# Performance work log

Hardware: AMD Instinct MI355X
Metric: run time of the kernel (lower is better)

Reference implementation:

```python
import jax, jax.numpy as jnp
import numpy as np

EPS = 1e-5


def gcn_conv(x, src, dst, W, b, n_nodes):
    # PyG GCNConv: linear first, symmetric normalization with self-loops.
    h = x @ W  # [N, out]
    deg = jnp.zeros((n_nodes,), h.dtype).at[dst].add(1.0) + 1.0  # +1 self-loop
    dinv = deg ** -0.5
    coef = dinv[src] * dinv[dst]  # [E]
    msg = h[src] * coef[:, None]  # edge gather (memory bound)
    agg = jax.ops.segment_sum(msg, dst, num_segments=n_nodes)
    agg = agg + h * (dinv * dinv)[:, None]  # self-loop term
    return agg + b


def graph_norm(x, batch, num_graphs, w, b, alpha):
    # PyG GraphNorm: per-graph mean/std with learnable mean scale alpha.
    ones = jnp.ones((x.shape[0],), x.dtype)
    cnt = jnp.maximum(jax.ops.segment_sum(ones, batch, num_segments=num_graphs), 1.0)
    mean = jax.ops.segment_sum(x, batch, num_segments=num_graphs) / cnt[:, None]
    out = x - alpha * mean[batch]
    var = jax.ops.segment_sum(out * out, batch, num_segments=num_graphs) / cnt[:, None]
    return w * out / jnp.sqrt(var + EPS)[batch] + b


def mean_pool(x, batch, num_graphs):
    ones = jnp.ones((x.shape[0],), x.dtype)
    cnt = jnp.maximum(jax.ops.segment_sum(ones, batch, num_segments=num_graphs), 1.0)
    return jax.ops.segment_sum(x, batch, num_segments=num_graphs) / cnt[:, None]


def setup_inputs() -> dict:
    key = jax.random.key(0)
    ks = jax.random.split(key, 16)
    N, E, G = 100000, 3200000, 512
    IN, H, OUT = 7, 128, 2
    x = jax.random.normal(ks[0], (N, IN), jnp.float32)
    edge_index = jax.random.randint(ks[1], (2, E), 0, N, jnp.int64)
    batch = jnp.sort(jax.random.randint(ks[2], (N,), 0, G, jnp.int64))
    s = lambda k, sh: jax.random.normal(k, sh, jnp.float32) * 0.05
    return {
        "x": x, "edge_index": edge_index, "batch": batch, "num_graphs": G,
        "W1": s(ks[3], (IN, H)), "b1": jnp.zeros((H,), jnp.float32),
        "gn1_w": jnp.ones((H,), jnp.float32), "gn1_b": jnp.zeros((H,), jnp.float32),
        "gn1_a": jnp.ones((H,), jnp.float32),
        "W2": s(ks[4], (H, H)), "b2": jnp.zeros((H,), jnp.float32),
        "gn2_w": jnp.ones((H,), jnp.float32), "gn2_b": jnp.zeros((H,), jnp.float32),
        "gn2_a": jnp.ones((H,), jnp.float32),
        "H1": s(ks[5], (H, H)), "hb1": jnp.zeros((H,), jnp.float32),
        "H2": s(ks[6], (H, OUT)), "hb2": jnp.zeros((OUT,), jnp.float32),
    }


def reference(x, edge_index, batch, num_graphs,
              W1, b1, gn1_w, gn1_b, gn1_a,
              W2, b2, gn2_w, gn2_b, gn2_a,
              H1, hb1, H2, hb2):
    n = x.shape[0]
    src, dst = edge_index[0], edge_index[1]
    # block 1
    h = gcn_conv(x, src, dst, W1, b1, n)
    h = graph_norm(h, batch, num_graphs, gn1_w, gn1_b, gn1_a)
    h = jax.nn.relu(h)
    # block 2
    h = gcn_conv(h, src, dst, W2, b2, n)
    h = graph_norm(h, batch, num_graphs, gn2_w, gn2_b, gn2_a)
    h = jax.nn.relu(h)
    # pool + MLP head (dropout inactive at eval)
    g = mean_pool(h, batch, num_graphs)  # [G, H]
    g = jax.nn.relu(g @ H1 + hb1)
    return g @ H2 + hb2  # [G, 2]
```

## Files before the change

### kernel.cpp

```cpp
#include <hip/hip_runtime.h>
#include <hip/hip_fp16.h>

#define EPSV 1e-5f
#define HDIM 128
#define BKT_SHIFT 9
#define BKT_SIZE 512
#define CHK 8192

typedef _Float16 f16x8 __attribute__((ext_vector_type(8)));
typedef float f32x4 __attribute__((ext_vector_type(4)));


__global__ __launch_bounds__(256) void hist_pass(const int* __restrict__ dst,
                                                 int* __restrict__ histG, int E, int NB) {
    __shared__ int h[BKT_SIZE];
    int t = threadIdx.x;
    for (int i = t; i < NB; i += 256) h[i] = 0;
    __syncthreads();
    int base = blockIdx.x * CHK;
    int end = min(base + CHK, E);
    for (int e = base + t; e < end; e += 256) atomicAdd(&h[dst[e] >> BKT_SHIFT], 1);
    __syncthreads();
    for (int i = t; i < NB; i += 256) histG[(size_t)blockIdx.x * NB + i] = h[i];
}

__global__ __launch_bounds__(512) void scan_chunks(int* __restrict__ histG,
                                                   int* __restrict__ tot,
                                                   int NCHUNK, int NB) {
    __shared__ int tmp[512];
    int b = blockIdx.x, t = threadIdx.x;
    int v = (t < NCHUNK) ? histG[(size_t)t * NB + b] : 0;
    tmp[t] = v;
    __syncthreads();
    for (int off = 1; off < 512; off <<= 1) {
        int x = (t >= off) ? tmp[t - off] : 0;
        __syncthreads();
        tmp[t] += x;
        __syncthreads();
    }
    if (t < NCHUNK) histG[(size_t)t * NB + b] = tmp[t] - v;
    if (t == 511) tot[b] = tmp[511];
}

__global__ __launch_bounds__(512) void scan_tot_k(const int* __restrict__ tot,
                                                  int* __restrict__ bucketBase,
                                                  int* __restrict__ rowStart,
                                                  int NB, int N, int E) {
    __shared__ int tmp[512];
    int t = threadIdx.x;
    int v = (t < NB) ? tot[t] : 0;
    tmp[t] = v;
    __syncthreads();
    for (int off = 1; off < 512; off <<= 1) {
        int x = (t >= off) ? tmp[t - off] : 0;
        __syncthreads();
        tmp[t] += x;
        __syncthreads();
    }
    if (t < NB) bucketBase[t] = tmp[t] - v;
    if (t == NB - 1) {
        bucketBase[NB] = tmp[t];
        rowStart[N] = E;
    }
}

__global__ __launch_bounds__(256) void add_base(int* __restrict__ histG,
                                                const int* __restrict__ bucketBase,
                                                int total, int NB) {
    int i = blockIdx.x * 256 + threadIdx.x;
    if (i < total) histG[i] += bucketBase[i % NB];
}

__global__ __launch_bounds__(256) void scatter_bkt(const int* __restrict__ src,
                                                   const int* __restrict__ dst,
                                                   const int* __restrict__ chunkOff,
                                                   unsigned int* __restrict__ EP,
                                                   int E, int NB) {
    __shared__ int cur[BKT_SIZE];
    int t = threadIdx.x, c = blockIdx.x;
    for (int i = t; i < NB; i += 256) cur[i] = chunkOff[(size_t)c * NB + i];
    __syncthreads();
    int base = c * CHK, end = min(base + CHK, E);
    for (int e = base + t; e < end; e += 256) {
        int d = dst[e];
        int b = d >> BKT_SHIFT;
        int pos = atomicAdd(&cur[b], 1);
        EP[pos] = (unsigned int)src[e] | ((unsigned int)(d & (BKT_SIZE - 1)) << 23);
    }
}

__global__ __launch_bounds__(512) void bucket_csr(const unsigned int* __restrict__ EP,
                                                  const int* __restrict__ bucketBase,
                                                  int* __restrict__ rowStart,
                                                  float* __restrict__ dinv,
                                                  int* __restrict__ col, int N) {
    __shared__ int cnt[BKT_SIZE];
    __shared__ int tmp[BKT_SIZE];
    int b = blockIdx.x, t = threadIdx.x;
    int ebase = bucketBase[b], eend = bucketBase[b + 1];
    cnt[t] = 0;
    __syncthreads();
    for (int e = ebase + t; e < eend; e += 512)
        atomicAdd(&cnt[(EP[e] >> 23) & 511], 1);
    __syncthreads();
    int v = cnt[t];
    tmp[t] = v;
    __syncthreads();
    for (int off = 1; off < 512; off <<= 1) {
        int x = (t >= off) ? tmp[t - off] : 0;
        __syncthreads();
        tmp[t] += x;
        __syncthreads();
    }
    int excl = tmp[t] - v;
    int n = (b << BKT_SHIFT) + t;
    if (n < N) {
        rowStart[n] = ebase + excl;
        dinv[n] = rsqrtf((float)v + 1.0f);
    }
    __syncthreads();
    cnt[t] = ebase + excl;
    __syncthreads();
    for (int e = ebase + t; e < eend; e += 512) {
        unsigned int p = EP[e];
        int ld = (p >> 23) & 511;
        int pos = atomicAdd(&cnt[ld], 1);
        col[pos] = (int)(p & 0x7FFFFFu);
    }
}

__device__ __forceinline__ int lbound(const int* __restrict__ b, int N, int key) {
    int lo = 0, hi = N;
    while (lo < hi) {
        int mid = (lo + hi) >> 1;
        if (b[mid] < key) lo = mid + 1; else hi = mid;
    }
    return lo;
}

__global__ __launch_bounds__(256) void graph_counts(const int* __restrict__ batch,
                                                    float* __restrict__ gcnt, int N, int G) {
    int g = blockIdx.x * 256 + threadIdx.x;
    if (g < G)
        gcnt[g] = (float)(lbound(batch, N, g + 1) - lbound(batch, N, g));
}

__global__ __launch_bounds__(256) void prep_w2t(const float* __restrict__ W2,
                                                __half* __restrict__ W2t) {
    int i = blockIdx.x * 256 + threadIdx.x;
    if (i < HDIM * HDIM) {
        int c = i >> 7, k = i & 127;
        W2t[c * HDIM + k] = __float2half(W2[k * HDIM + c]);
    }
}

__global__ __launch_bounds__(256) void prep_xs(const float* __restrict__ x,
                                               const float* __restrict__ dinv,
                                               float* __restrict__ xs, long long total) {
    long long idx = (long long)blockIdx.x * 256 + threadIdx.x;
    if (idx >= total) return;
    int n = (int)(idx >> 3), k = (int)(idx & 7);
    xs[idx] = (k < 7) ? x[(long long)n * 7 + k] * dinv[n] : 0.f;
}

__global__ __launch_bounds__(256) void agg7k(const int* __restrict__ col,
                                             const int* __restrict__ rowStart,
                                             const float* __restrict__ xs,
                                             float* __restrict__ agg, int N) {
    int wib = threadIdx.x >> 6, lane = threadIdx.x & 63;
    int stream = lane >> 2;
    int c2 = (lane & 3) * 2;
    int n = blockIdx.x * 4 + wib;
    if (n >= N) return;
    float2 acc = make_float2(0.f, 0.f);
    int rs = rowStart[n], re = rowStart[n + 1];
    if (stream == 0) acc = *(const float2*)(xs + (size_t)n * 8 + c2);
    int j = rs + stream;
    for (; j + 16 < re; j += 32) {
        int e0 = col[j], e1 = col[j + 16];
        float2 r0 = *(const float2*)(xs + (size_t)e0 * 8 + c2);
        float2 r1 = *(const float2*)(xs + (size_t)e1 * 8 + c2);
        acc.x += r0.x + r1.x;
        acc.y += r0.y + r1.y;
    }
    for (; j < re; j += 16) {
        float2 r = *(const float2*)(xs + (size_t)col[j] * 8 + c2);
        acc.x += r.x; acc.y += r.y;
    }
#pragma unroll
    for (int off = 4; off <= 32; off <<= 1) {
        acc.x += __shfl_xor(acc.x, off);
        acc.y += __shfl_xor(acc.y, off);
    }
    if (stream == 0) *(float2*)(agg + (size_t)n * 8 + c2) = acc;
}

__global__ __launch_bounds__(512) void l1post(const float* __restrict__ agg,
                                              const float* __restrict__ W1,
                                              const float* __restrict__ b1,
                                              const float* __restrict__ dinv,
                                              __half* __restrict__ A16, int N) {
    __shared__ float w1s[7 * HDIM];
    int t = threadIdx.x;
    for (int i = t; i < 7 * HDIM; i += 512) w1s[i] = W1[i];
    int wib = t >> 7, c = t & 127;
    int n = blockIdx.x * 4 + wib;
    __syncthreads();
    if (n < N) {
        const float* ar = agg + (size_t)n * 8;
        float s = 0.f;
#pragma unroll
        for (int k = 0; k < 7; k++) s += ar[k] * w1s[k * HDIM + c];
        A16[(size_t)n * HDIM + c] = __float2half(s * dinv[n] + b1[c]);
    }
}

__global__ __launch_bounds__(256) void stats2(const __half* __restrict__ X,
                                              const int* __restrict__ batch,
                                              float* __restrict__ gsum,
                                              float* __restrict__ gsq, int N) {
    int t = threadIdx.x;
    int c = t & 127;
    int half_ = t >> 7;
    int n0 = blockIdx.x * 32;
    float s = 0.f, q = 0.f;
    int cur = -1;
    for (int i = half_; i < 32; i += 2) {
        int n = n0 + i;
        if (n >= N) break;
        int b = batch[n];
        if (b != cur) {
            if (cur >= 0) {
                unsafeAtomicAdd(&gsum[(size_t)cur * HDIM + c], s);
                unsafeAtomicAdd(&gsq[(size_t)cur * HDIM + c], q);
            }
            cur = b; s = 0.f; q = 0.f;
        }
        float v = __half2float(X[(size_t)n * HDIM + c]);
        s += v; q += v * v;
    }
    if (cur >= 0) {
        unsafeAtomicAdd(&gsum[(size_t)cur * HDIM + c], s);
        unsafeAtomicAdd(&gsq[(size_t)cur * HDIM + c], q);
    }
}

__global__ __launch_bounds__(256) void gstat(float* __restrict__ gsum,
                                             float* __restrict__ gsq,
                                             const float* __restrict__ gcnt,
                                             const float* __restrict__ alpha, int total) {
    int i = blockIdx.x * 256 + threadIdx.x;
    if (i < total) {
        int g = i >> 7, c = i & 127;
        float cnt = fmaxf(gcnt[g], 1.f);
        float mean = gsum[i] / cnt;
        float m2 = gsq[i] / cnt;
        float a = alpha[c];
        float var = m2 + mean * mean * (a * a - 2.f * a);
        gsum[i] = mean;
        gsq[i] = rsqrtf(fmaxf(var, 0.f) + EPSV);
    }
}

__global__ __launch_bounds__(256) void mm_h_mfma(const __half* __restrict__ A16,
                                                 const float* __restrict__ gmean,
                                                 const float* __restrict__ gistd,
                                                 const float* __restrict__ alpha,
                                                 const float* __restrict__ w,
                                                 const float* __restrict__ bb,
                                                 const int* __restrict__ batch,
                                                 const __half* __restrict__ W2t,
                                                 const float* __restrict__ dinv,
                                                 __half* __restrict__ Q, int N) {
    __shared__ _Float16 XS[64][136];
    __shared__ _Float16 WT[HDIM][136];
    __shared__ float pA[HDIM], pW[HDIM], pB[HDIM];
    int t = threadIdx.x;
    for (int i = t; i < HDIM; i += 256) { pA[i] = alpha[i]; pW[i] = w[i]; pB[i] = bb[i]; }
    int n0 = blockIdx.x * 64;

    for (int i = t; i < HDIM * 16; i += 256) {
        int row = i >> 4;
        int kk = (i & 15) * 8;
        *(uint4*)&WT[row][kk] = *(const uint4*)(W2t + (size_t)row * HDIM + kk);
    }
    __syncthreads();

    for (int i = t; i < 64 * 16; i += 256) {
        int nn = i >> 4;
        int kk = (i & 15) * 8;
        int gn = n0 + nn;
        __half hv[8];
#pragma unroll
        for (int k = 0; k < 8; k++) hv[k] = __float2half(0.f);
        if (gn < N) {
            uint4 u = *(const uint4*)(A16 + (size_t)gn * HDIM + kk);
            int b = batch[gn];
            const float* mp = gmean + (size_t)b * HDIM + kk;
            const float* ip = gistd + (size_t)b * HDIM + kk;
            float2 f0 = __half22float2(*(__half2*)&u.x);
            float2 f1 = __half22float2(*(__half2*)&u.y);
            float2 f2 = __half22float2(*(__half2*)&u.z);
            float2 f3 = __half22float2(*(__half2*)&u.w);
            float f[8] = {f0.x, f0.y, f1.x, f1.y, f2.x, f2.y, f3.x, f3.y};
#pragma unroll
            for (int k = 0; k < 8; k++) {
                int c = kk + k;
                hv[k] = __float2half(fmaxf(pW[c] * (f[k] - pA[c] * mp[k]) * ip[k] + pB[c], 0.f));
            }
        }
        *(uint4*)&XS[nn][kk] = *(uint4*)hv;
    }
    __syncthreads();

    int wid = t >> 6, lane = t & 63;
    int m0 = wid * 16;
    int rlane = lane & 15;
    int kgrp = lane >> 4;
    f32x4 acc[8];
#pragma unroll
    for (int ct = 0; ct < 8; ct++) acc[ct] = (f32x4){0.f, 0.f, 0.f, 0.f};

#pragma unroll
    for (int kt = 0; kt < 4; ++kt) {
        int kbase = kt * 32 + kgrp * 8;
        f16x8 a = *(const f16x8*)&XS[m0 + rlane][kbase];
#pragma unroll
        for (int ct = 0; ct < 8; ++ct) {
            f16x8 bfr = *(const f16x8*)&WT[ct * 16 + rlane][kbase];
            acc[ct] = __builtin_amdgcn_mfma_f32_16x16x32_f16(a, bfr, acc[ct], 0, 0, 0);
        }
    }

    int rgrp = lane >> 4;
    float dv[4];
    int gnr[4];
#pragma unroll
    for (int r = 0; r < 4; r++) {
        gnr[r] = n0 + m0 + rgrp * 4 + r;
        dv[r] = (gnr[r] < N) ? dinv[gnr[r]] : 0.f;
    }
#pragma unroll
    for (int ct = 0; ct < 8; ++ct) {
#pragma unroll
        for (int r = 0; r < 4; ++r) {
            if (gnr[r] < N)
                Q[(size_t)gnr[r] * HDIM + ct * 16 + rlane] = __float2half(acc[ct][r] * dv[r]);
        }
    }
}

__device__ __forceinline__ float4 qrow4(const __half* __restrict__ Q, int e, int c4) {
    uint2 u = *(const uint2*)(Q + (size_t)e * HDIM + c4);
    float2 f0 = __half22float2(*(__half2*)&u.x);
    float2 f1 = __half22float2(*(__half2*)&u.y);
    return make_float4(f0.x, f0.y, f1.x, f1.y);
}

__global__ __launch_bounds__(256) void node_agg2(const int* __restrict__ col,
                                                 const int* __restrict__ rowStart,
                                                 const __half* __restrict__ Q,
                                                 const float* __restrict__ dinv,
                                                 const float* __restrict__ bias,
                                                 __half* __restrict__ A2, int N) {
    int wib = threadIdx.x >> 6;
    int lane = threadIdx.x & 63;
    int half = lane >> 5;
    int l = lane & 31;
    int c4 = l * 4;
    int n = blockIdx.x * 4 + wib;
    if (n >= N) return;
    float4 acc = make_float4(0.f, 0.f, 0.f, 0.f);
    int rs = rowStart[n], re = rowStart[n + 1];
    if (half == 0) acc = qrow4(Q, n, c4);
    int j = rs + half;
    for (; j + 14 < re; j += 16) {
        int e0 = col[j],      e1 = col[j + 2],  e2 = col[j + 4],  e3 = col[j + 6];
        int e4 = col[j + 8],  e5 = col[j + 10], e6 = col[j + 12], e7 = col[j + 14];
        float4 r0 = qrow4(Q, e0, c4);
        float4 r1 = qrow4(Q, e1, c4);
        float4 r2 = qrow4(Q, e2, c4);
        float4 r3 = qrow4(Q, e3, c4);
        float4 r4 = qrow4(Q, e4, c4);
        float4 r5 = qrow4(Q, e5, c4);
        float4 r6 = qrow4(Q, e6, c4);
        float4 r7 = qrow4(Q, e7, c4);
        acc.x += ((r0.x + r1.x) + (r2.x + r3.x)) + ((r4.x + r5.x) + (r6.x + r7.x));
        acc.y += ((r0.y + r1.y) + (r2.y + r3.y)) + ((r4.y + r5.y) + (r6.y + r7.y));
        acc.z += ((r0.z + r1.z) + (r2.z + r3.z)) + ((r4.z + r5.z) + (r6.z + r7.z));
        acc.w += ((r0.w + r1.w) + (r2.w + r3.w)) + ((r4.w + r5.w) + (r6.w + r7.w));
    }
    for (; j + 6 < re; j += 8) {
        int e0 = col[j], e1 = col[j + 2], e2 = col[j + 4], e3 = col[j + 6];
        float4 r0 = qrow4(Q, e0, c4);
        float4 r1 = qrow4(Q, e1, c4);
        float4 r2 = qrow4(Q, e2, c4);
        float4 r3 = qrow4(Q, e3, c4);
        acc.x += (r0.x + r1.x) + (r2.x + r3.x);
        acc.y += (r0.y + r1.y) + (r2.y + r3.y);
        acc.z += (r0.z + r1.z) + (r2.z + r3.z);
        acc.w += (r0.w + r1.w) + (r2.w + r3.w);
    }
    for (; j < re; j += 2) {
        float4 r = qrow4(Q, col[j], c4);
        acc.x += r.x; acc.y += r.y; acc.z += r.z; acc.w += r.w;
    }
    acc.x += __shfl_xor(acc.x, 32);
    acc.y += __shfl_xor(acc.y, 32);
    acc.z += __shfl_xor(acc.z, 32);
    acc.w += __shfl_xor(acc.w, 32);
    if (half == 0) {
        float dv = dinv[n];
        acc.x = acc.x * dv + bias[c4];
        acc.y = acc.y * dv + bias[c4 + 1];
        acc.z = acc.z * dv + bias[c4 + 2];
        acc.w = acc.w * dv + bias[c4 + 3];
        __half2 o0 = __floats2half2_rn(acc.x, acc.y);
        __half2 o1 = __floats2half2_rn(acc.z, acc.w);
        uint2 u;
        u.x = *(unsigned int*)&o0;
        u.y = *(unsigned int*)&o1;
        *(uint2*)(A2 + (size_t)n * HDIM + c4) = u;
    }
}

__global__ __launch_bounds__(256) void node_norm_pool(const __half* __restrict__ A2,
                                                      const float* __restrict__ gmean,
                                                      const float* __restrict__ gistd,
                                                      const float* __restrict__ alpha,
                                                      const float* __restrict__ w,
                                                      const float* __restrict__ bb,
                                                      const int* __restrict__ batch,
                                                      float* __restrict__ gpool, int N) {
    int t = threadIdx.x;
    int c = t & 127;
    int half_ = t >> 7;
    int n0 = blockIdx.x * 32;
    float ac = alpha[c], wc = w[c], bc = bb[c];
    float s = 0.f, mc = 0.f, ic = 0.f;
    int cur = -1;
    for (int i = half_; i < 32; i += 2) {
        int n = n0 + i;
        if (n >= N) break;
        int b = batch[n];
        if (b != cur) {
            if (cur >= 0) unsafeAtomicAdd(&gpool[(size_t)cur * HDIM + c], s);
            cur = b; s = 0.f;
            mc = gmean[(size_t)b * HDIM + c];
            ic = gistd[(size_t)b * HDIM + c];
        }
        float v = __half2float(A2[(size_t)n * HDIM + c]);
        s += fmaxf(wc * (v - ac * mc) * ic + bc, 0.f);
    }
    if (cur >= 0) unsafeAtomicAdd(&gpool[(size_t)cur * HDIM + c], s);
}

__global__ __launch_bounds__(128) void head(const float* __restrict__ gpool,
                                            const float* __restrict__ gcnt,
                                            const float* __restrict__ H1,
                                            const float* __restrict__ hb1,
                                            const float* __restrict__ H2,
                                            const float* __restrict__ hb2,
                                            float* __restrict__ out, int G) {
    __shared__ float gv[HDIM];
    __shared__ float tv[HDIM];
    __shared__ float r0[HDIM], r1[HDIM];
    int g = blockIdx.x;
    int c = threadIdx.x;
    float cnt = fmaxf(gcnt[g], 1.0f);
    gv[c] = gpool[(long long)g * HDIM + c] / cnt;
    __syncthreads();
    float s = hb1[c];
    for (int k = 0; k < HDIM; k++) s += gv[k] * H1[k * HDIM + c];
    tv[c] = fmaxf(s, 0.f);
    __syncthreads();
    r0[c] = tv[c] * H2[c * 2 + 0];
    r1[c] = tv[c] * H2[c * 2 + 1];
    __syncthreads();
    for (int off = 64; off > 0; off >>= 1) {
        if (c < off) { r0[c] += r0[c + off]; r1[c] += r1[c + off]; }
        __syncthreads();
    }
    if (c == 0) {
        out[(long long)g * 2 + 0] = r0[0] + hb2[0];
        out[(long long)g * 2 + 1] = r1[0] + hb2[1];
    }
}

extern "C" void kernel_launch(void* const* d_in, const int* in_sizes, int n_in,
                              void* d_out, int out_size, void* d_ws, size_t ws_size,
                              hipStream_t stream) {
    const float* x    = (const float*)d_in[0];
    const int*   ei   = (const int*)d_in[1];
    const int*   batch= (const int*)d_in[2];
    const float* W1   = (const float*)d_in[4];
    const float* b1   = (const float*)d_in[5];
    const float* gn1w = (const float*)d_in[6];
    const float* gn1b = (const float*)d_in[7];
    const float* gn1a = (const float*)d_in[8];
    const float* W2   = (const float*)d_in[9];
    const float* b2   = (const float*)d_in[10];
    const float* gn2w = (const float*)d_in[11];
    const float* gn2b = (const float*)d_in[12];
    const float* gn2a = (const float*)d_in[13];
    const float* H1   = (const float*)d_in[14];
    const float* hb1  = (const float*)d_in[15];
    const float* H2   = (const float*)d_in[16];
    const float* hb2  = (const float*)d_in[17];

    int N = in_sizes[0] / 7;
    int E = in_sizes[1] / 2;
    int G = out_size / 2;
    const int* srcI = ei;
    const int* dstI = ei + E;

    int NB = (N + BKT_SIZE - 1) >> BKT_SHIFT;
    int NCHUNK = (E + CHK - 1) / CHK;

    __half* A16   = (__half*)d_ws;
    __half* A2    = A16;
    __half* Q16   = A16 + (size_t)N * HDIM;
    float*  xs    = (float*)(Q16 + (size_t)N * HDIM);
    float*  agg   = xs + (size_t)N * 8;
    float*  gsum1 = agg + (size_t)N * 8;
    float*  gsq1  = gsum1 + (size_t)G * HDIM;
    float*  gsum2 = gsq1 + (size_t)G * HDIM;
    float*  gsq2  = gsum2 + (size_t)G * HDIM;
    float*  gpool = gsq2 + (size_t)G * HDIM;
    float*  gcnt  = gpool + (size_t)G * HDIM;
    float*  dinv  = gcnt + G;
    int* rowStart = (int*)(dinv + N);
    unsigned int* EP = (unsigned int*)(rowStart + N + 2);
    int* col      = (int*)(EP + E);
    int* histG    = col + E;
    int* tot      = histG + (size_t)NCHUNK * NB;
    int* bucketBase = tot + NB + 2;
    __half* W2t   = (__half*)(bucketBase + NB + 2);

    int gridNW = (N + 3) / 4;
    int gridGH = (G * HDIM + 255) / 256;
    int gridMM = (N + 63) / 64;
    int gridNS = (N + 31) / 32;

    hipMemsetAsync(gsum1, 0, (size_t)G * HDIM * 5 * 4, stream);

    hist_pass<<<NCHUNK, 256, 0, stream>>>(dstI, histG, E, NB);
    scan_chunks<<<NB, 512, 0, stream>>>(histG, tot, NCHUNK, NB);
    scan_tot_k<<<1, 512, 0, stream>>>(tot, bucketBase, rowStart, NB, N, E);
    add_base<<<((NCHUNK * NB) + 255) / 256, 256, 0, stream>>>(histG, bucketBase, NCHUNK * NB, NB);
    scatter_bkt<<<NCHUNK, 256, 0, stream>>>(srcI, dstI, histG, EP, E, NB);
    bucket_csr<<<NB, 512, 0, stream>>>(EP, bucketBase, rowStart, dinv, col, N);

    graph_counts<<<(G + 255) / 256, 256, 0, stream>>>(batch, gcnt, N, G);

    prep_w2t<<<(HDIM * HDIM + 255) / 256, 256, 0, stream>>>(W2, W2t);

    long long nx8 = (long long)N * 8;
    prep_xs<<<(int)((nx8 + 255) / 256), 256, 0, stream>>>(x, dinv, xs, nx8);
    agg7k<<<gridNW, 256, 0, stream>>>(col, rowStart, xs, agg, N);
    l1post<<<gridNW, 512, 0, stream>>>(agg, W1, b1, dinv, A16, N);
    stats2<<<gridNS, 256, 0, stream>>>(A16, batch, gsum1, gsq1, N);
    gstat<<<gridGH, 256, 0, stream>>>(gsum1, gsq1, gcnt, gn1a, G * HDIM);

    mm_h_mfma<<<gridMM, 256, 0, stream>>>(A16, gsum1, gsq1, gn1a, gn1w, gn1b, batch,
                                          W2t, dinv, Q16, N);

    node_agg2<<<gridNW, 256, 0, stream>>>(col, rowStart, Q16, dinv, b2, A2, N);
    stats2<<<gridNS, 256, 0, stream>>>(A2, batch, gsum2, gsq2, N);
    gstat<<<gridGH, 256, 0, stream>>>(gsum2, gsq2, gcnt, gn2a, G * HDIM);

    node_norm_pool<<<gridNS, 256, 0, stream>>>(A2, gsum2, gsq2, gn2a, gn2w, gn2b, batch, gpool, N);

    head<<<G, 128, 0, stream>>>(gpool, gcnt, H1, hb1, H2, hb2, (float*)d_out, G);
}
```

Before: 373.7 us.

## Shrink CSR buckets and chunks, fuse layer-1 aggregation with W1 projection

Halves the bucket size to 256 destination nodes and the edge chunk to 4096, so there are more buckets and chunks. This gives the bucket CSR build more blocks and less shared-memory contention per block, at the cost of a wider chunk scan with 1024-thread blocks. Fuses the 7-wide neighbor aggregation with the W1 projection, which removes the intermediate agg buffer and one launch. It also merges the graph-count and W2-transpose setup kernels into one launch.

```diff
diff --git a/kernel.cpp b/kernel.cpp
--- a/kernel.cpp
+++ b/kernel.cpp
@@ -3,9 +3,10 @@
 
 #define EPSV 1e-5f
 #define HDIM 128
-#define BKT_SHIFT 9
-#define BKT_SIZE 512
-#define CHK 8192
+#define BKT_SHIFT 8
+#define BKT_SIZE 256
+#define NBMAX 512
+#define CHK 4096
 
 typedef _Float16 f16x8 __attribute__((ext_vector_type(8)));
 typedef float f32x4 __attribute__((ext_vector_type(4)));
@@ -13,7 +14,7 @@
 
 __global__ __launch_bounds__(256) void hist_pass(const int* __restrict__ dst,
                                                  int* __restrict__ histG, int E, int NB) {
-    __shared__ int h[BKT_SIZE];
+    __shared__ int h[NBMAX];
     int t = threadIdx.x;
     for (int i = t; i < NB; i += 256) h[i] = 0;
     __syncthreads();
@@ -24,22 +25,22 @@
     for (int i = t; i < NB; i += 256) histG[(size_t)blockIdx.x * NB + i] = h[i];
 }
 
-__global__ __launch_bounds__(512) void scan_chunks(int* __restrict__ histG,
-                                                   int* __restrict__ tot,
-                                                   int NCHUNK, int NB) {
-    __shared__ int tmp[512];
+__global__ __launch_bounds__(1024) void scan_chunks(int* __restrict__ histG,
+                                                    int* __restrict__ tot,
+                                                    int NCHUNK, int NB) {
+    __shared__ int tmp[1024];
     int b = blockIdx.x, t = threadIdx.x;
     int v = (t < NCHUNK) ? histG[(size_t)t * NB + b] : 0;
     tmp[t] = v;
     __syncthreads();
-    for (int off = 1; off < 512; off <<= 1) {
+    for (int off = 1; off < 1024; off <<= 1) {
         int x = (t >= off) ? tmp[t - off] : 0;
         __syncthreads();
         tmp[t] += x;
         __syncthreads();
     }
     if (t < NCHUNK) histG[(size_t)t * NB + b] = tmp[t] - v;
-    if (t == 511) tot[b] = tmp[511];
+    if (t == 1023) tot[b] = tmp[1023];
 }
 
 __global__ __launch_bounds__(512) void scan_tot_k(const int* __restrict__ tot,
@@ -76,7 +77,7 @@
                                                    const int* __restrict__ chunkOff,
                                                    unsigned int* __restrict__ EP,
                                                    int E, int NB) {
-    __shared__ int cur[BKT_SIZE];
+    __shared__ int cur[NBMAX];
     int t = threadIdx.x, c = blockIdx.x;
     for (int i = t; i < NB; i += 256) cur[i] = chunkOff[(size_t)c * NB + i];
     __syncthreads();
@@ -98,33 +99,33 @@
     __shared__ int tmp[BKT_SIZE];
     int b = blockIdx.x, t = threadIdx.x;
     int ebase = bucketBase[b], eend = bucketBase[b + 1];
-    cnt[t] = 0;
+    if (t < BKT_SIZE) cnt[t] = 0;
     __syncthreads();
     for (int e = ebase + t; e < eend; e += 512)
-        atomicAdd(&cnt[(EP[e] >> 23) & 511], 1);
-    __syncthreads();
-    int v = cnt[t];
-    tmp[t] = v;
-    __syncthreads();
-    for (int off = 1; off < 512; off <<= 1) {
-        int x = (t >= off) ? tmp[t - off] : 0;
-        __syncthreads();
-        tmp[t] += x;
-        __syncthreads();
-    }
-    int excl = tmp[t] - v;
-    int n = (b << BKT_SHIFT) + t;
-    if (n < N) {
-        rowStart[n] = ebase + excl;
-        dinv[n] = rsqrtf((float)v + 1.0f);
-    }
-    __syncthreads();
-    cnt[t] = ebase + excl;
+        atomicAdd(&cnt[(EP[e] >> 23) & (BKT_SIZE - 1)], 1);
+    __syncthreads();
+    int v = (t < BKT_SIZE) ? cnt[t] : 0;
+    if (t < BKT_SIZE) tmp[t] = v;
+    __syncthreads();
+    for (int off = 1; off < BKT_SIZE; off <<= 1) {
+        int x = (t >= off && t < BKT_SIZE) ? tmp[t - off] : 0;
+        __syncthreads();
+        if (t < BKT_SIZE) tmp[t] += x;
+        __syncthreads();
+    }
+    if (t < BKT_SIZE) {
+        int excl = tmp[t] - v;
+        int n = (b << BKT_SHIFT) + t;
+        if (n < N) {
+            rowStart[n] = ebase + excl;
+            dinv[n] = rsqrtf((float)v + 1.0f);
+        }
+        cnt[t] = ebase + excl;
+    }
     __syncthreads();
     for (int e = ebase + t; e < eend; e += 512) {
         unsigned int p = EP[e];
-        int ld = (p >> 23) & 511;
-        int pos = atomicAdd(&cnt[ld], 1);
+        int pos = atomicAdd(&cnt[(p >> 23) & (BKT_SIZE - 1)], 1);
         col[pos] = (int)(p & 0x7FFFFFu);
     }
 }
@@ -138,19 +139,17 @@
     return lo;
 }
 
-__global__ __launch_bounds__(256) void graph_counts(const int* __restrict__ batch,
-                                                    float* __restrict__ gcnt, int N, int G) {
-    int g = blockIdx.x * 256 + threadIdx.x;
-    if (g < G)
-        gcnt[g] = (float)(lbound(batch, N, g + 1) - lbound(batch, N, g));
-}
-
-__global__ __launch_bounds__(256) void prep_w2t(const float* __restrict__ W2,
-                                                __half* __restrict__ W2t) {
+__global__ __launch_bounds__(256) void setup_misc(const float* __restrict__ W2,
+                                                  __half* __restrict__ W2t,
+                                                  const int* __restrict__ batch,
+                                                  float* __restrict__ gcnt, int N, int G) {
     int i = blockIdx.x * 256 + threadIdx.x;
     if (i < HDIM * HDIM) {
         int c = i >> 7, k = i & 127;
         W2t[c * HDIM + k] = __float2half(W2[k * HDIM + c]);
+    } else if (i - HDIM * HDIM < G) {
+        int g = i - HDIM * HDIM;
+        gcnt[g] = (float)(lbound(batch, N, g + 1) - lbound(batch, N, g));
     }
 }
 
@@ -163,55 +162,59 @@
     xs[idx] = (k < 7) ? x[(long long)n * 7 + k] * dinv[n] : 0.f;
 }
 
-__global__ __launch_bounds__(256) void agg7k(const int* __restrict__ col,
+__global__ __launch_bounds__(256) void aggl1(const int* __restrict__ col,
                                              const int* __restrict__ rowStart,
                                              const float* __restrict__ xs,
-                                             float* __restrict__ agg, int N) {
-    int wib = threadIdx.x >> 6, lane = threadIdx.x & 63;
+                                             const float* __restrict__ W1,
+                                             const float* __restrict__ b1,
+                                             const float* __restrict__ dinv,
+                                             __half* __restrict__ A16, int N) {
+    __shared__ float w1s[7 * HDIM];
+    __shared__ float aggs[4][8];
+    int t = threadIdx.x;
+    for (int i = t; i < 7 * HDIM; i += 256) w1s[i] = W1[i];
+    int wib = t >> 6, lane = t & 63;
     int stream = lane >> 2;
     int c2 = (lane & 3) * 2;
     int n = blockIdx.x * 4 + wib;
-    if (n >= N) return;
     float2 acc = make_float2(0.f, 0.f);
-    int rs = rowStart[n], re = rowStart[n + 1];
-    if (stream == 0) acc = *(const float2*)(xs + (size_t)n * 8 + c2);
-    int j = rs + stream;
-    for (; j + 16 < re; j += 32) {
-        int e0 = col[j], e1 = col[j + 16];
-        float2 r0 = *(const float2*)(xs + (size_t)e0 * 8 + c2);
-        float2 r1 = *(const float2*)(xs + (size_t)e1 * 8 + c2);
-        acc.x += r0.x + r1.x;
-        acc.y += r0.y + r1.y;
-    }
-    for (; j < re; j += 16) {
-        float2 r = *(const float2*)(xs + (size_t)col[j] * 8 + c2);
-        acc.x += r.x; acc.y += r.y;
-    }
-#pragma unroll
-    for (int off = 4; off <= 32; off <<= 1) {
-        acc.x += __shfl_xor(acc.x, off);
-        acc.y += __shfl_xor(acc.y, off);
-    }
-    if (stream == 0) *(float2*)(agg + (size_t)n * 8 + c2) = acc;
-}
-
-__global__ __launch_bounds__(512) void l1post(const float* __restrict__ agg,
-                                              const float* __restrict__ W1,
-                                              const float* __restrict__ b1,
-                                              const float* __restrict__ dinv,
-                                              __half* __restrict__ A16, int N) {
-    __shared__ float w1s[7 * HDIM];
-    int t = threadIdx.x;
-    for (int i = t; i < 7 * HDIM; i += 512) w1s[i] = W1[i];
-    int wib = t >> 7, c = t & 127;
-    int n = blockIdx.x * 4 + wib;
-    __syncthreads();
     if (n < N) {
-        const float* ar = agg + (size_t)n * 8;
-        float s = 0.f;
-#pragma unroll
-        for (int k = 0; k < 7; k++) s += ar[k] * w1s[k * HDIM + c];
-        A16[(size_t)n * HDIM + c] = __float2half(s * dinv[n] + b1[c]);
+        int rs = rowStart[n], re = rowStart[n + 1];
+        if (stream == 0) acc = *(const float2*)(xs + (size_t)n * 8 + c2);
+        int j = rs + stream;
+        for (; j + 16 < re; j += 32) {
+            int e0 = col[j], e1 = col[j + 16];
+            float2 r0 = *(const float2*)(xs + (size_t)e0 * 8 + c2);
+            float2 r1 = *(const float2*)(xs + (size_t)e1 * 8 + c2);
+            acc.x += r0.x + r1.x;
+            acc.y += r0.y + r1.y;
+        }
+        for (; j < re; j += 16) {
+            float2 r = *(const float2*)(xs + (size_t)col[j] * 8 + c2);
+            acc.x += r.x; acc.y += r.y;
+        }
+#pragma unroll
+        for (int off = 4; off <= 32; off <<= 1) {
+            acc.x += __shfl_xor(acc.x, off);
+            acc.y += __shfl_xor(acc.y, off);
+        }
+        if (stream == 0) { aggs[wib][c2] = acc.x; aggs[wib][c2 + 1] = acc.y; }
+    }
+    __syncthreads();
+    if (n < N) {
+        float ar[7];
+#pragma unroll
+        for (int k = 0; k < 7; k++) ar[k] = aggs[wib][k];
+        float dv = dinv[n];
+        int c = lane * 2;
+        float s0 = 0.f, s1 = 0.f;
+#pragma unroll
+        for (int k = 0; k < 7; k++) {
+            s0 += ar[k] * w1s[k * HDIM + c];
+            s1 += ar[k] * w1s[k * HDIM + c + 1];
+        }
+        *(__half2*)(A16 + (size_t)n * HDIM + c) =
+            __floats2half2_rn(s0 * dv + b1[c], s1 * dv + b1[c + 1]);
     }
 }
 
@@ -521,8 +524,7 @@
     __half* A2    = A16;
     __half* Q16   = A16 + (size_t)N * HDIM;
     float*  xs    = (float*)(Q16 + (size_t)N * HDIM);
-    float*  agg   = xs + (size_t)N * 8;
-    float*  gsum1 = agg + (size_t)N * 8;
+    float*  gsum1 = xs + (size_t)N * 8;
     float*  gsq1  = gsum1 + (size_t)G * HDIM;
     float*  gsum2 = gsq1 + (size_t)G * HDIM;
     float*  gsq2  = gsum2 + (size_t)G * HDIM;
@@ -545,20 +547,17 @@
     hipMemsetAsync(gsum1, 0, (size_t)G * HDIM * 5 * 4, stream);
 
     hist_pass<<<NCHUNK, 256, 0, stream>>>(dstI, histG, E, NB);
-    scan_chunks<<<NB, 512, 0, stream>>>(histG, tot, NCHUNK, NB);
+    scan_chunks<<<NB, 1024, 0, stream>>>(histG, tot, NCHUNK, NB);
     scan_tot_k<<<1, 512, 0, stream>>>(tot, bucketBase, rowStart, NB, N, E);
     add_base<<<((NCHUNK * NB) + 255) / 256, 256, 0, stream>>>(histG, bucketBase, NCHUNK * NB, NB);
     scatter_bkt<<<NCHUNK, 256, 0, stream>>>(srcI, dstI, histG, EP, E, NB);
     bucket_csr<<<NB, 512, 0, stream>>>(EP, bucketBase, rowStart, dinv, col, N);
 
-    graph_counts<<<(G + 255) / 256, 256, 0, stream>>>(batch, gcnt, N, G);
-
-    prep_w2t<<<(HDIM * HDIM + 255) / 256, 256, 0, stream>>>(W2, W2t);
+    setup_misc<<<(HDIM * HDIM + G + 255) / 256, 256, 0, stream>>>(W2, W2t, batch, gcnt, N, G);
 
     long long nx8 = (long long)N * 8;
     prep_xs<<<(int)((nx8 + 255) / 256), 256, 0, stream>>>(x, dinv, xs, nx8);
-    agg7k<<<gridNW, 256, 0, stream>>>(col, rowStart, xs, agg, N);
-    l1post<<<gridNW, 512, 0, stream>>>(agg, W1, b1, dinv, A16, N);
+    aggl1<<<gridNW, 256, 0, stream>>>(col, rowStart, xs, W1, b1, dinv, A16, N);
     stats2<<<gridNS, 256, 0, stream>>>(A16, batch, gsum1, gsq1, N);
     gstat<<<gridGH, 256, 0, stream>>>(gsum1, gsq1, gcnt, gn1a, G * HDIM);
 
```

Result: faster. 354.4 us (-5.2%).
